# Kernel optimization log

Hardware: AMD Instinct MI355X
Metric: run time of the kernel (lower is better)

## Reference

```python
import jax, jax.numpy as jnp
import numpy as np

E = 8          # num_experts
TOP_K = 2      # num_selects
D = 2048       # hidden_size
F_E = 8192 // E  # per-expert intermediate size
EPS = 1e-6
SCALE = E / TOP_K


def setup_inputs() -> dict:
    key = jax.random.key(0)
    ks = jax.random.split(key, 6)
    B, S = 2, 2048
    std = 0.02
    return {
        "hidden_states": jax.random.normal(ks[0], (B, S, D), jnp.float32),
        "router_w": jax.random.normal(ks[1], (E, D), jnp.float32) * std,   # Linear(D->E).weight
        "norm_w": jnp.ones((D,), jnp.float32),                               # RMSNorm weight
        "gate_w": jax.random.normal(ks[2], (E, D, F_E), jnp.float32) * std,  # per-expert gate_proj
        "up_w": jax.random.normal(ks[3], (E, D, F_E), jnp.float32) * std,    # per-expert up_proj
        "down_w": jax.random.normal(ks[4], (E, F_E, D), jnp.float32) * std,  # per-expert down_proj
    }


def reference(hidden_states, router_w, norm_w, gate_w, up_w, down_w):
    B, S, Dm = hidden_states.shape
    T = B * S
    flat = hidden_states.reshape(T, Dm)

    # RMSNorm (fp32 math) used ONLY for the router input
    xf = flat.astype(jnp.float32)
    var = jnp.mean(xf * xf, axis=-1, keepdims=True)
    router_in = norm_w * (xf * jax.lax.rsqrt(var + EPS)).astype(flat.dtype)

    # Router: softmax over experts, top-k, renormalize
    logits = router_in @ router_w.T                    # [T, E]
    probs = jax.nn.softmax(logits, axis=-1)
    topw, topi = jax.lax.top_k(probs, TOP_K)           # [T, k]
    topw = topw / jnp.sum(topw, axis=-1, keepdims=True)

    # Dense combine weights: zero for non-selected (token, expert) pairs,
    # so the dense expert evaluation below matches the masked gather/scatter math.
    cw = jnp.zeros((T, E), flat.dtype).at[jnp.arange(T)[:, None], topi].add(topw)

    # Experts receive the RAW flat hidden (not the normalized router input)
    g = jnp.einsum('td,edf->tef', flat, gate_w)        # [T, E, F_E]
    u = jnp.einsum('td,edf->tef', flat, up_w)
    a = jax.nn.silu(g) * u
    expert_out = jnp.einsum('tef,efd->ted', a, down_w) # [T, E, D]

    y = jnp.einsum('ted,te->td', expert_out, cw) * SCALE
    return y.reshape(B, S, Dm)
```

## Files before the change

### kernel.cpp

```cpp
#include <hip/hip_runtime.h>
#include <hip/hip_bf16.h>


#define TOK 4096
#define DIM 2048
#define NE 8
#define FE 1024
#define SCALE_F 4.0f
#define BK 32

typedef __bf16 bf16x8 __attribute__((ext_vector_type(8)));
typedef __bf16 bf16x4 __attribute__((ext_vector_type(4)));
typedef float f32x4 __attribute__((ext_vector_type(4)));

__device__ __forceinline__ void gll16(const void* g, void* l) {
  __builtin_amdgcn_global_load_lds(
      (const __attribute__((address_space(1))) unsigned int*)g,
      (__attribute__((address_space(3))) unsigned int*)l, 16, 0, 0);
}

#define MFMA16(a, b, c) __builtin_amdgcn_mfma_f32_16x16x32_bf16((a), (b), (c), 0, 0, 0)
#define VMCNT4 asm volatile("s_waitcnt vmcnt(4)" ::: "memory")
#define VMCNT0 asm volatile("s_waitcnt vmcnt(0)" ::: "memory")
#define LGKM0  asm volatile("s_waitcnt lgkmcnt(0)" ::: "memory")
#define SCHED0 __builtin_amdgcn_sched_barrier(0)
#define BAR    __builtin_amdgcn_s_barrier()

__global__ __launch_bounds__(256) void k_fused_cvt_router(
    const float* __restrict__ x, const float* __restrict__ rw,
    const float* __restrict__ nwt, __bf16* __restrict__ xbf,
    int* __restrict__ topi, float* __restrict__ topw,
    const float* __restrict__ gw, const float* __restrict__ uw,
    const float* __restrict__ dwp, __bf16* __restrict__ gwt,
    __bf16* __restrict__ uwt, __bf16* __restrict__ dwt) {
  __shared__ __align__(16) __bf16 lt[128][136];
  int tid = threadIdx.x;

  if (blockIdx.x < TOK) {
    int t = blockIdx.x;
    const float* xr = x + (size_t)t * DIM;
    float ssq = 0.f;
    float pe[NE];
#pragma unroll
    for (int e = 0; e < NE; ++e) pe[e] = 0.f;

#pragma unroll
    for (int i = 0; i < 2; ++i) {
      int c4 = tid + i * 256;
      float4 v = ((const float4*)xr)[c4];
      int c = c4 * 4;
      bf16x4 b;
      b[0] = (__bf16)v.x; b[1] = (__bf16)v.y; b[2] = (__bf16)v.z; b[3] = (__bf16)v.w;
      *(bf16x4*)(xbf + (size_t)t * DIM + c) = b;
      float m0 = nwt[c + 0] * v.x, m1 = nwt[c + 1] * v.y;
      float m2 = nwt[c + 2] * v.z, m3 = nwt[c + 3] * v.w;
      ssq += v.x * v.x + v.y * v.y + v.z * v.z + v.w * v.w;
#pragma unroll
      for (int e = 0; e < NE; ++e) {
        float4 rv = ((const float4*)(rw + (size_t)e * DIM))[c4];
        pe[e] += m0 * rv.x + m1 * rv.y + m2 * rv.z + m3 * rv.w;
      }
    }
#pragma unroll
    for (int off = 32; off > 0; off >>= 1) {
      ssq += __shfl_down(ssq, off);
#pragma unroll
      for (int e = 0; e < NE; ++e) pe[e] += __shfl_down(pe[e], off);
    }
    float (*red)[NE + 1] = (float (*)[NE + 1])&lt[0][0];
    int wid = tid >> 6, lane = tid & 63;
    if (lane == 0) {
      red[wid][0] = ssq;
#pragma unroll
      for (int e = 0; e < NE; ++e) red[wid][1 + e] = pe[e];
    }
    __syncthreads();
    if (tid == 0) {
      float s = red[0][0] + red[1][0] + red[2][0] + red[3][0];
      float rs = rsqrtf(s / (float)DIM + 1e-6f);
      float l[NE];
#pragma unroll
      for (int e = 0; e < NE; ++e)
        l[e] = (red[0][1 + e] + red[1][1 + e] + red[2][1 + e] + red[3][1 + e]) * rs;
      int i1 = 0;
#pragma unroll
      for (int e = 1; e < NE; ++e) if (l[e] > l[i1]) i1 = e;
      int i2 = -1;
#pragma unroll
      for (int e = 0; e < NE; ++e) if (e != i1 && (i2 < 0 || l[e] > l[i2])) i2 = e;
      float e2 = __expf(l[i2] - l[i1]);
      float inv = 1.f / (1.f + e2);
      topi[2 * t] = i1; topi[2 * t + 1] = i2;
      topw[2 * t] = inv; topw[2 * t + 1] = e2 * inv;
    }
  } else {
    int bx = blockIdx.x - TOK;
    int m = bx >> 7;
    int tilex = bx & 127;
    int which = m >> 3, e = m & 7;
    const float* src; __bf16* dst; int K, N;
    if (which == 0)      { src = gw;  dst = gwt; K = DIM; N = FE; }
    else if (which == 1) { src = uw;  dst = uwt; K = DIM; N = FE; }
    else                 { src = dwp; dst = dwt; K = FE;  N = DIM; }
    src += (size_t)e * K * N;
    dst += (size_t)e * K * N;
    int tiles_n = N / 128;
    int k0 = (tilex / tiles_n) * 128, n0c = (tilex % tiles_n) * 128;

#pragma unroll
    for (int p = 0; p < 16; ++p) {
      int idx = tid + p * 256;
      int row = idx >> 5, c4 = idx & 31;
      float4 v = *(const float4*)(src + (size_t)(k0 + row) * N + n0c + c4 * 4);
      int cc = c4 * 4;
      lt[cc + 0][row] = (__bf16)v.x;
      lt[cc + 1][row] = (__bf16)v.y;
      lt[cc + 2][row] = (__bf16)v.z;
      lt[cc + 3][row] = (__bf16)v.w;
    }
    __syncthreads();
    int kblocks = K >> 5;
    int n_ = tid >> 2, kc = tid & 3;
#pragma unroll
    for (int q = 0; q < 8; ++q) {
      int bn = q >> 2, bk = q & 3;
      size_t blk = ((size_t)((n0c >> 6) + bn) * kblocks + (k0 >> 5) + bk) * 2048;
      bf16x8 w = *(const bf16x8*)&lt[bn * 64 + n_][bk * 32 + kc * 8];
      *(bf16x8*)(dst + blk + n_ * 32 + kc * 8) = w;
    }
  }
}

__global__ __launch_bounds__(256) void k_prefix_place(
    int* __restrict__ offsets, const int* __restrict__ topi,
    const float* __restrict__ topw, int* __restrict__ row_token,
    float* __restrict__ row_wt, int* __restrict__ invp) {
  __shared__ int hist[4][NE];
  __shared__ int lcur[NE];
  int tid = threadIdx.x, wid = tid >> 6;
  if (tid < 4 * NE) ((int*)hist)[tid] = 0;
  __syncthreads();
  for (int i = tid; i < 2 * TOK; i += 256)
    atomicAdd(&hist[wid][topi[i]], 1);
  __syncthreads();
  if (tid == 0) {
    int acc = 0;
    for (int e = 0; e < NE; ++e) {
      int c = hist[0][e] + hist[1][e] + hist[2][e] + hist[3][e];
      offsets[e] = acc;
      lcur[e] = acc;
      acc += c;
    }
    offsets[NE] = acc;
  }
  __syncthreads();
  for (int t = tid; t < TOK; t += 256) {
#pragma unroll
    for (int s = 0; s < 2; ++s) {
      int e = topi[2 * t + s];
      int pos = atomicAdd(&lcur[e], 1);
      row_token[pos] = t;
      row_wt[pos] = topw[2 * t + s] * SCALE_F;
      invp[2 * t + s] = pos;
    }
  }
}

__global__ __launch_bounds__(256) void k_combine(
    const __bf16* __restrict__ dbuf, const float* __restrict__ topw,
    const int* __restrict__ invp, float* __restrict__ out) {
  int t = blockIdx.x;
  int c = threadIdx.x * 8;
  int p0 = invp[2 * t], p1 = invp[2 * t + 1];
  float w0 = topw[2 * t] * SCALE_F, w1 = topw[2 * t + 1] * SCALE_F;
  bf16x8 a = *(const bf16x8*)(dbuf + (size_t)p0 * DIM + c);
  bf16x8 b = *(const bf16x8*)(dbuf + (size_t)p1 * DIM + c);
  float4 o0, o1;
  o0.x = w0 * (float)a[0] + w1 * (float)b[0];
  o0.y = w0 * (float)a[1] + w1 * (float)b[1];
  o0.z = w0 * (float)a[2] + w1 * (float)b[2];
  o0.w = w0 * (float)a[3] + w1 * (float)b[3];
  o1.x = w0 * (float)a[4] + w1 * (float)b[4];
  o1.y = w0 * (float)a[5] + w1 * (float)b[5];
  o1.z = w0 * (float)a[6] + w1 * (float)b[6];
  o1.w = w0 * (float)a[7] + w1 * (float)b[7];
  *(float4*)(out + (size_t)t * DIM + c) = o0;
  *(float4*)(out + (size_t)t * DIM + c + 4) = o1;
}


__global__ __launch_bounds__(256) void k_gateup16(
    const __bf16* __restrict__ xbf, const __bf16* __restrict__ gwt,
    const __bf16* __restrict__ uwt, const int* __restrict__ row_token,
    const int* __restrict__ offsets, __bf16* __restrict__ abuf) {
  int lin = blockIdx.x;
  int nw = (lin & 7) * 512 + (lin >> 3);
  int ytile = nw & 31, xt = (nw >> 5) & 15, e = nw >> 9;
  int row_start = offsets[e], row_end = offsets[e + 1];
  int tile_row = row_start + ytile * 128;
  if (tile_row >= row_end) return;
  int n0 = xt * 64;

  __shared__ __align__(16) __bf16 As0[128][BK], As1[128][BK];
  __shared__ __align__(16) __bf16 Bg0[64][BK],  Bg1[64][BK];
  __shared__ __align__(16) __bf16 Bu0[64][BK],  Bu1[64][BK];
  __shared__ int toks[128];

  int tid = threadIdx.x;
  if (tid < 128) {
    int r = tile_row + tid;
    toks[tid] = (r < row_end) ? row_token[r] : row_token[row_start];
  }
  __syncthreads();

  int wid = tid >> 6, lane = tid & 63;
  int lrow = lane >> 2;
  int lke = (((lane & 3) ^ ((lane >> 3) & 3)) * 8);
  int lks = (((lane >> 4) ^ ((lane >> 1) & 3)) * 8);

  const __bf16* pa0 = xbf + (size_t)toks[wid * 32 + lrow] * DIM + lke;
  const __bf16* pa1 = xbf + (size_t)toks[wid * 32 + 16 + lrow] * DIM + lke;
  const __bf16* pg = gwt + (size_t)e * FE * DIM + (size_t)xt * 64 * 2048 +
                     (wid * 16 + lrow) * 32 + lke;
  const __bf16* pu = uwt + (size_t)e * FE * DIM + (size_t)xt * 64 * 2048 +
                     (wid * 16 + lrow) * 32 + lke;

  f32x4 accg[4][2], accu[4][2];
#pragma unroll
  for (int i = 0; i < 4; ++i)
#pragma unroll
    for (int j = 0; j < 2; ++j) { accg[i][j] = (f32x4)0.f; accu[i][j] = (f32x4)0.f; }

  int lr = lane & 15;
  int wm = (wid >> 1) * 64, wn = (wid & 1) * 32;

  bf16x8 af0, af1, af2, af3, bgv0, bgv1, buv0, buv1;

#define GU_STAGE(AS, BG, BU)                                 \
  do {                                                       \
    gll16(pa0, (void*)&AS[wid * 32][0]);                     \
    gll16(pa1, (void*)&AS[wid * 32 + 16][0]);                \
    gll16(pg, (void*)&BG[wid * 16][0]);                      \
    gll16(pu, (void*)&BU[wid * 16][0]);                      \
    pa0 += BK; pa1 += BK; pg += 2048; pu += 2048;            \
  } while (0)

#define GU_LOAD(AS, BG, BU)                                  \
  do {                                                       \
    af0 = *(const bf16x8*)&AS[wm + lr][lks];                 \
    af1 = *(const bf16x8*)&AS[wm + 16 + lr][lks];            \
    af2 = *(const bf16x8*)&AS[wm + 32 + lr][lks];            \
    af3 = *(const bf16x8*)&AS[wm + 48 + lr][lks];            \
    bgv0 = *(const bf16x8*)&BG[wn + lr][lks];                \
    bgv1 = *(const bf16x8*)&BG[wn + 16 + lr][lks];           \
    buv0 = *(const bf16x8*)&BU[wn + lr][lks];                \
    buv1 = *(const bf16x8*)&BU[wn + 16 + lr][lks];           \
  } while (0)

#define GU_MFMA()                                            \
  do {                                                       \
    __builtin_amdgcn_s_setprio(1);                           \
    accg[0][0] = MFMA16(af0, bgv0, accg[0][0]);              \
    accg[0][1] = MFMA16(af0, bgv1, accg[0][1]);              \
    accu[0][0] = MFMA16(af0, buv0, accu[0][0]);              \
    accu[0][1] = MFMA16(af0, buv1, accu[0][1]);              \
    accg[1][0] = MFMA16(af1, bgv0, accg[1][0]);              \
    accg[1][1] = MFMA16(af1, bgv1, accg[1][1]);              \
    accu[1][0] = MFMA16(af1, buv0, accu[1][0]);              \
    accu[1][1] = MFMA16(af1, buv1, accu[1][1]);              \
    accg[2][0] = MFMA16(af2, bgv0, accg[2][0]);              \
    accg[2][1] = MFMA16(af2, bgv1, accg[2][1]);              \
    accu[2][0] = MFMA16(af2, buv0, accu[2][0]);              \
    accu[2][1] = MFMA16(af2, buv1, accu[2][1]);              \
    accg[3][0] = MFMA16(af3, bgv0, accg[3][0]);              \
    accg[3][1] = MFMA16(af3, bgv1, accg[3][1]);              \
    accu[3][0] = MFMA16(af3, buv0, accu[3][0]);              \
    accu[3][1] = MFMA16(af3, buv1, accu[3][1]);              \
    __builtin_amdgcn_s_setprio(0);                           \
  } while (0)

  GU_STAGE(As0, Bg0, Bu0);
  GU_STAGE(As1, Bg1, Bu1);
#pragma unroll 1
  for (int it = 0; it < 31; ++it) {
    VMCNT4; BAR;
    GU_LOAD(As0, Bg0, Bu0);
    LGKM0; SCHED0; BAR;
    GU_STAGE(As0, Bg0, Bu0);
    GU_MFMA();
    VMCNT4; BAR;
    GU_LOAD(As1, Bg1, Bu1);
    LGKM0; SCHED0; BAR;
    GU_STAGE(As1, Bg1, Bu1);
    GU_MFMA();
  }
  VMCNT4; BAR;
  GU_LOAD(As0, Bg0, Bu0);
  GU_MFMA();
  VMCNT0; BAR;
  GU_LOAD(As1, Bg1, Bu1);
  GU_MFMA();
#undef GU_STAGE
#undef GU_LOAD
#undef GU_MFMA

  int rowq = (lane >> 4) * 4;
  f32x4* ag = &accg[0][0];
  f32x4* au = &accu[0][0];
#pragma unroll
  for (int mi = 0; mi < 4; ++mi) {
#pragma unroll
    for (int ni = 0; ni < 2; ++ni) {
#pragma unroll
      for (int j = 0; j < 4; ++j) {
        int rg = tile_row + wm + mi * 16 + rowq + j;
        if (rg < row_end) {
          float g = ag[mi * 2 + ni][j], u = au[mi * 2 + ni][j];
          float sig = 1.f / (1.f + __expf(-g));
          abuf[(size_t)rg * FE + n0 + wn + ni * 16 + lr] = (__bf16)(g * sig * u);
        }
      }
    }
  }
}

__global__ __launch_bounds__(256) void k_down16(
    const __bf16* __restrict__ abuf, const __bf16* __restrict__ dwt,
    const int* __restrict__ offsets, __bf16* __restrict__ dbuf) {
  int lin = blockIdx.x;
  int nw = (lin & 7) * 512 + (lin >> 3);
  int ytile = nw & 31, xt = (nw >> 5) & 15, e = nw >> 9;
  int row_start = offsets[e], row_end = offsets[e + 1];
  int tile_row = row_start + ytile * 128;
  if (tile_row >= row_end) return;
  int n0 = xt * 128;

  __shared__ __align__(16) __bf16 As0[128][BK], As1[128][BK];
  __shared__ __align__(16) __bf16 Bs0[128][BK], Bs1[128][BK];

  int tid = threadIdx.x;
  int wid = tid >> 6, lane = tid & 63;
  int lrow = lane >> 2;
  int lke = (((lane & 3) ^ ((lane >> 3) & 3)) * 8);
  int lks = (((lane >> 4) ^ ((lane >> 1) & 3)) * 8);

  const __bf16* pa0 = abuf + (size_t)(tile_row + wid * 32 + lrow) * FE + lke;
  const __bf16* pa1 = pa0 + (size_t)16 * FE;
  const __bf16* pb0 = dwt + (size_t)e * DIM * FE +
                      ((size_t)(2 * xt + (wid >> 1)) * 32) * 2048 +
                      ((wid & 1) * 32 + lrow) * 32 + lke;
  const __bf16* pb1 = pb0 + 16 * 32;

  f32x4 acc[4][4];
#pragma unroll
  for (int i = 0; i < 4; ++i)
#pragma unroll
    for (int j = 0; j < 4; ++j) acc[i][j] = (f32x4)0.f;

  int lr = lane & 15;
  int wm = (wid >> 1) * 64, wn = (wid & 1) * 64;

  bf16x8 af0, af1, af2, af3, bb0, bb1, bb2, bb3;

#define DN_STAGE(AS, BS)                                     \
  do {                                                       \
    gll16(pa0, (void*)&AS[wid * 32][0]);                     \
    gll16(pa1, (void*)&AS[wid * 32 + 16][0]);                \
    gll16(pb0, (void*)&BS[wid * 32][0]);                     \
    gll16(pb1, (void*)&BS[wid * 32 + 16][0]);                \
    pa0 += BK; pa1 += BK; pb0 += 2048; pb1 += 2048;          \
  } while (0)

#define DN_LOAD(AS, BS)                                      \
  do {                                                       \
    af0 = *(const bf16x8*)&AS[wm + lr][lks];                 \
    af1 = *(const bf16x8*)&AS[wm + 16 + lr][lks];            \
    af2 = *(const bf16x8*)&AS[wm + 32 + lr][lks];            \
    af3 = *(const bf16x8*)&AS[wm + 48 + lr][lks];            \
    bb0 = *(const bf16x8*)&BS[wn + lr][lks];                 \
    bb1 = *(const bf16x8*)&BS[wn + 16 + lr][lks];            \
    bb2 = *(const bf16x8*)&BS[wn + 32 + lr][lks];            \
    bb3 = *(const bf16x8*)&BS[wn + 48 + lr][lks];            \
  } while (0)

#define DN_MFMA()                                            \
  do {                                                       \
    __builtin_amdgcn_s_setprio(1);                           \
    acc[0][0] = MFMA16(af0, bb0, acc[0][0]);                 \
    acc[1][0] = MFMA16(af1, bb0, acc[1][0]);                 \
    acc[2][0] = MFMA16(af2, bb0, acc[2][0]);                 \
    acc[3][0] = MFMA16(af3, bb0, acc[3][0]);                 \
    acc[0][1] = MFMA16(af0, bb1, acc[0][1]);                 \
    acc[1][1] = MFMA16(af1, bb1, acc[1][1]);                 \
    acc[2][1] = MFMA16(af2, bb1, acc[2][1]);                 \
    acc[3][1] = MFMA16(af3, bb1, acc[3][1]);                 \
    acc[0][2] = MFMA16(af0, bb2, acc[0][2]);                 \
    acc[1][2] = MFMA16(af1, bb2, acc[1][2]);                 \
    acc[2][2] = MFMA16(af2, bb2, acc[2][2]);                 \
    acc[3][2] = MFMA16(af3, bb2, acc[3][2]);                 \
    acc[0][3] = MFMA16(af0, bb3, acc[0][3]);                 \
    acc[1][3] = MFMA16(af1, bb3, acc[1][3]);                 \
    acc[2][3] = MFMA16(af2, bb3, acc[2][3]);                 \
    acc[3][3] = MFMA16(af3, bb3, acc[3][3]);                 \
    __builtin_amdgcn_s_setprio(0);                           \
  } while (0)

  DN_STAGE(As0, Bs0);
  DN_STAGE(As1, Bs1);
#pragma unroll 1
  for (int it = 0; it < 15; ++it) {
    VMCNT4; BAR;
    DN_LOAD(As0, Bs0);
    LGKM0; SCHED0; BAR;
    DN_STAGE(As0, Bs0);
    DN_MFMA();
    VMCNT4; BAR;
    DN_LOAD(As1, Bs1);
    LGKM0; SCHED0; BAR;
    DN_STAGE(As1, Bs1);
    DN_MFMA();
  }
  VMCNT4; BAR;
  DN_LOAD(As0, Bs0);
  DN_MFMA();
  VMCNT0; BAR;
  DN_LOAD(As1, Bs1);
  DN_MFMA();
#undef DN_STAGE
#undef DN_LOAD
#undef DN_MFMA

  int rowq = (lane >> 4) * 4;
#pragma unroll
  for (int mi = 0; mi < 4; ++mi) {
#pragma unroll
    for (int j = 0; j < 4; ++j) {
      int rg = tile_row + wm + mi * 16 + rowq + j;
      if (rg < row_end) {
#pragma unroll
        for (int ni = 0; ni < 4; ++ni) {
          dbuf[(size_t)rg * DIM + n0 + wn + ni * 16 + lr] = (__bf16)acc[mi][ni][j];
        }
      }
    }
  }
}


#define PAD 8
__global__ __launch_bounds__(256) void k_gateup_fb(
    const __bf16* __restrict__ xbf, const float* __restrict__ gw,
    const float* __restrict__ uw, const int* __restrict__ row_token,
    const int* __restrict__ offsets, __bf16* __restrict__ abuf) {
  int e = blockIdx.z;
  int row_start = offsets[e], row_end = offsets[e + 1];
  int tile_row = row_start + blockIdx.y * 128;
  if (tile_row >= row_end) return;
  int n0 = blockIdx.x * 128;

  __shared__ __align__(16) __bf16 As[128][BK + PAD];
  __shared__ __align__(16) __bf16 Bgs[128][BK + PAD];
  __shared__ __align__(16) __bf16 Bus[128][BK + PAD];
  __shared__ int toks[128];

  int tid = threadIdx.x;
  if (tid < 128) {
    int r = tile_row + tid;
    toks[tid] = (r < row_end) ? row_token[r] : row_token[row_start];
  }
  __syncthreads();

  f32x4 accg[4][4]; f32x4 accu[4][4];
#pragma unroll
  for (int i = 0; i < 4; ++i)
#pragma unroll
    for (int j = 0; j < 4; ++j) { accg[i][j] = (f32x4)0.f; accu[i][j] = (f32x4)0.f; }

  int wid = tid >> 6, lane = tid & 63;
  int wm = (wid >> 1) * 64, wn = (wid & 1) * 64;
  int lr = lane & 15, lk = (lane >> 4) * 8;

  const float* gbase = gw + (size_t)e * DIM * FE + n0;
  const float* ubase = uw + (size_t)e * DIM * FE + n0;
  int n4 = (tid & 31) * 4;
  int kb = tid >> 5;

  for (int k0 = 0; k0 < DIM; k0 += BK) {
#pragma unroll
    for (int p = 0; p < 2; ++p) {
      int g = tid + p * 256;
      int r = g >> 2, kk = (g & 3) * 8;
      *(bf16x8*)&As[r][kk] = *(const bf16x8*)(xbf + (size_t)toks[r] * DIM + k0 + kk);
    }
#pragma unroll
    for (int p = 0; p < 4; ++p) {
      int k = kb + p * 8;
      const float4 vg = *(const float4*)(gbase + (size_t)(k0 + k) * FE + n4);
      const float4 vu = *(const float4*)(ubase + (size_t)(k0 + k) * FE + n4);
      Bgs[n4 + 0][k] = (__bf16)vg.x; Bgs[n4 + 1][k] = (__bf16)vg.y;
      Bgs[n4 + 2][k] = (__bf16)vg.z; Bgs[n4 + 3][k] = (__bf16)vg.w;
      Bus[n4 + 0][k] = (__bf16)vu.x; Bus[n4 + 1][k] = (__bf16)vu.y;
      Bus[n4 + 2][k] = (__bf16)vu.z; Bus[n4 + 3][k] = (__bf16)vu.w;
    }
    __syncthreads();

    bf16x8 af[4];
#pragma unroll
    for (int mi = 0; mi < 4; ++mi)
      af[mi] = *(const bf16x8*)&As[wm + mi * 16 + lr][lk];
#pragma unroll
    for (int ni = 0; ni < 4; ++ni) {
      bf16x8 bg = *(const bf16x8*)&Bgs[wn + ni * 16 + lr][lk];
      bf16x8 bu = *(const bf16x8*)&Bus[wn + ni * 16 + lr][lk];
#pragma unroll
      for (int mi = 0; mi < 4; ++mi) {
        accg[mi][ni] = MFMA16(af[mi], bg, accg[mi][ni]);
        accu[mi][ni] = MFMA16(af[mi], bu, accu[mi][ni]);
      }
    }
    __syncthreads();
  }

  int rowq = (lane >> 4) * 4;
#pragma unroll
  for (int mi = 0; mi < 4; ++mi) {
#pragma unroll
    for (int ni = 0; ni < 4; ++ni) {
#pragma unroll
      for (int j = 0; j < 4; ++j) {
        int rg = tile_row + wm + mi * 16 + rowq + j;
        if (rg < row_end) {
          float g = accg[mi][ni][j], u = accu[mi][ni][j];
          float sig = 1.f / (1.f + __expf(-g));
          abuf[(size_t)rg * FE + n0 + wn + ni * 16 + lr] = (__bf16)(g * sig * u);
        }
      }
    }
  }
}

__global__ __launch_bounds__(256) void k_down_fb(
    const __bf16* __restrict__ abuf, const float* __restrict__ dw,
    const int* __restrict__ row_token, const float* __restrict__ row_wt,
    const int* __restrict__ offsets, float* __restrict__ out) {
  int e = blockIdx.z;
  int row_start = offsets[e], row_end = offsets[e + 1];
  int tile_row = row_start + blockIdx.y * 128;
  if (tile_row >= row_end) return;
  int n0 = blockIdx.x * 128;

  __shared__ __align__(16) __bf16 As[128][BK + PAD];
  __shared__ __align__(16) __bf16 Bs[128][BK + PAD];

  int tid = threadIdx.x;
  f32x4 acc[4][4];
#pragma unroll
  for (int i = 0; i < 4; ++i)
#pragma unroll
    for (int j = 0; j < 4; ++j) acc[i][j] = (f32x4)0.f;

  int wid = tid >> 6, lane = tid & 63;
  int wm = (wid >> 1) * 64, wn = (wid & 1) * 64;
  int lr = lane & 15, lk = (lane >> 4) * 8;

  const float* dbase = dw + (size_t)e * FE * DIM + n0;
  int n4 = (tid & 31) * 4;
  int kb = tid >> 5;

  for (int k0 = 0; k0 < FE; k0 += BK) {
#pragma unroll
    for (int p = 0; p < 2; ++p) {
      int g = tid + p * 256;
      int r = g >> 2, kk = (g & 3) * 8;
      *(bf16x8*)&As[r][kk] = *(const bf16x8*)(abuf + (size_t)(tile_row + r) * FE + k0 + kk);
    }
#pragma unroll
    for (int p = 0; p < 4; ++p) {
      int k = kb + p * 8;
      const float4 vb = *(const float4*)(dbase + (size_t)(k0 + k) * DIM + n4);
      Bs[n4 + 0][k] = (__bf16)vb.x; Bs[n4 + 1][k] = (__bf16)vb.y;
      Bs[n4 + 2][k] = (__bf16)vb.z; Bs[n4 + 3][k] = (__bf16)vb.w;
    }
    __syncthreads();

    bf16x8 af[4];
#pragma unroll
    for (int mi = 0; mi < 4; ++mi)
      af[mi] = *(const bf16x8*)&As[wm + mi * 16 + lr][lk];
#pragma unroll
    for (int ni = 0; ni < 4; ++ni) {
      bf16x8 bb = *(const bf16x8*)&Bs[wn + ni * 16 + lr][lk];
#pragma unroll
      for (int mi = 0; mi < 4; ++mi)
        acc[mi][ni] = MFMA16(af[mi], bb, acc[mi][ni]);
    }
    __syncthreads();
  }

  int rowq = (lane >> 4) * 4;
#pragma unroll
  for (int mi = 0; mi < 4; ++mi) {
#pragma unroll
    for (int j = 0; j < 4; ++j) {
      int rg = tile_row + wm + mi * 16 + rowq + j;
      if (rg < row_end) {
        int tok = row_token[rg];
        float w = row_wt[rg];
#pragma unroll
        for (int ni = 0; ni < 4; ++ni) {
          atomicAdd(&out[(size_t)tok * DIM + n0 + wn + ni * 16 + lr],
                    acc[mi][ni][j] * w);
        }
      }
    }
  }
}

extern "C" void kernel_launch(void* const* d_in, const int* in_sizes, int n_in,
                              void* d_out, int out_size, void* d_ws, size_t ws_size,
                              hipStream_t stream) {
  const float* x  = (const float*)d_in[0];
  const float* rw = (const float*)d_in[1];
  const float* nw = (const float*)d_in[2];
  const float* gw = (const float*)d_in[3];
  const float* uw = (const float*)d_in[4];
  const float* dwp= (const float*)d_in[5];
  float* out = (float*)d_out;

  char* p = (char*)d_ws;
  int* offsets   = (int*)(p + 64);
  int* topi      = (int*)(p + 256);
  float* topw    = (float*)(p + 256 + 32768);
  int* row_token = (int*)(p + 256 + 65536);
  float* row_wt  = (float*)(p + 256 + 98304);
  int* invp      = (int*)(p + 256 + 131072);
  __bf16* xbf    = (__bf16*)(p + 256 + 163840);
  __bf16* abuf   = xbf + (size_t)TOK * DIM;
  __bf16* gwt    = abuf + ((size_t)2 * TOK + 128) * FE;
  __bf16* uwt    = gwt + (size_t)NE * DIM * FE;
  __bf16* dwt    = uwt + (size_t)NE * DIM * FE;
  __bf16* dbuf   = gwt;

  size_t need = 256 + 163840 +
                ((size_t)TOK * DIM + ((size_t)2 * TOK + 128) * FE) * 2 +
                3 * (size_t)NE * DIM * FE * 2;
  bool fast = ws_size >= need;

  if (!fast)
    hipMemsetAsync(d_out, 0, (size_t)TOK * DIM * sizeof(float), stream);

  if (fast) {
    k_fused_cvt_router<<<TOK + 3072, 256, 0, stream>>>(
        x, rw, nw, xbf, topi, topw, gw, uw, dwp, gwt, uwt, dwt);
    k_prefix_place<<<1, 256, 0, stream>>>(offsets, topi, topw,
                                          row_token, row_wt, invp);
    k_gateup16<<<4096, 256, 0, stream>>>(xbf, gwt, uwt, row_token, offsets, abuf);
    k_down16<<<4096, 256, 0, stream>>>(abuf, dwt, offsets, dbuf);
    k_combine<<<TOK, 256, 0, stream>>>(dbuf, topw, invp, out);
  } else {
    k_fused_cvt_router<<<TOK, 256, 0, stream>>>(
        x, rw, nw, xbf, topi, topw, gw, uw, dwp, gwt, uwt, dwt);
    k_prefix_place<<<1, 256, 0, stream>>>(offsets, topi, topw,
                                          row_token, row_wt, invp);
    k_gateup_fb<<<dim3(FE / 128, 32, NE), 256, 0, stream>>>(xbf, gw, uw, row_token, offsets, abuf);
    k_down_fb<<<dim3(DIM / 128, 32, NE), 256, 0, stream>>>(abuf, dwp, row_token, row_wt, offsets, out);
  }
}
```

Measured before the change: 254.2 us.

## Load expert weight fragments directly into registers, bypassing LDS staging

The gate/up and down grouped GEMMs now read B (weight) MFMA fragments straight from global memory into registers, double-buffered across iterations, instead of staging them through LDS. Only the gathered activation tile still goes through LDS, and the vmcnt wait depth is raised to cover the extra in-flight register loads. This is meant to cut LDS traffic, LDS footprint and ds_read pressure. In exchange each wave loads its own B fragments with no sharing across waves, which raises global/L2 traffic and VGPR usage.

```diff
diff --git a/kernel.cpp b/kernel.cpp
--- a/kernel.cpp
+++ b/kernel.cpp
@@ -20,7 +20,7 @@
 }
 
 #define MFMA16(a, b, c) __builtin_amdgcn_mfma_f32_16x16x32_bf16((a), (b), (c), 0, 0, 0)
-#define VMCNT4 asm volatile("s_waitcnt vmcnt(4)" ::: "memory")
+#define VMCNT6 asm volatile("s_waitcnt vmcnt(6)" ::: "memory")
 #define VMCNT0 asm volatile("s_waitcnt vmcnt(0)" ::: "memory")
 #define LGKM0  asm volatile("s_waitcnt lgkmcnt(0)" ::: "memory")
 #define SCHED0 __builtin_amdgcn_sched_barrier(0)
@@ -189,7 +189,7 @@
 }
 
 
-__global__ __launch_bounds__(256) void k_gateup16(
+__global__ __launch_bounds__(256) void k_gateup18(
     const __bf16* __restrict__ xbf, const __bf16* __restrict__ gwt,
     const __bf16* __restrict__ uwt, const int* __restrict__ row_token,
     const int* __restrict__ offsets, __bf16* __restrict__ abuf) {
@@ -202,8 +202,6 @@
   int n0 = xt * 64;
 
   __shared__ __align__(16) __bf16 As0[128][BK], As1[128][BK];
-  __shared__ __align__(16) __bf16 Bg0[64][BK],  Bg1[64][BK];
-  __shared__ __align__(16) __bf16 Bu0[64][BK],  Bu1[64][BK];
   __shared__ int toks[128];
 
   int tid = threadIdx.x;
@@ -220,88 +218,102 @@
 
   const __bf16* pa0 = xbf + (size_t)toks[wid * 32 + lrow] * DIM + lke;
   const __bf16* pa1 = xbf + (size_t)toks[wid * 32 + 16 + lrow] * DIM + lke;
-  const __bf16* pg = gwt + (size_t)e * FE * DIM + (size_t)xt * 64 * 2048 +
-                     (wid * 16 + lrow) * 32 + lke;
-  const __bf16* pu = uwt + (size_t)e * FE * DIM + (size_t)xt * 64 * 2048 +
-                     (wid * 16 + lrow) * 32 + lke;
-
-  f32x4 accg[4][2], accu[4][2];
-#pragma unroll
-  for (int i = 0; i < 4; ++i)
-#pragma unroll
-    for (int j = 0; j < 2; ++j) { accg[i][j] = (f32x4)0.f; accu[i][j] = (f32x4)0.f; }
 
   int lr = lane & 15;
   int wm = (wid >> 1) * 64, wn = (wid & 1) * 32;
-
-  bf16x8 af0, af1, af2, af3, bgv0, bgv1, buv0, buv1;
-
-#define GU_STAGE(AS, BG, BU)                                 \
+  int chunk = (lane >> 4) * 8;
+
+  const __bf16* pgB = gwt + (size_t)e * FE * DIM + (size_t)xt * 64 * 2048 +
+                      (wn + lr) * 32 + chunk;
+  const __bf16* puB = uwt + (size_t)e * FE * DIM + (size_t)xt * 64 * 2048 +
+                      (wn + lr) * 32 + chunk;
+
+  f32x4 accg[4][2], accu[4][2];
+#pragma unroll
+  for (int i = 0; i < 4; ++i)
+#pragma unroll
+    for (int j = 0; j < 2; ++j) { accg[i][j] = (f32x4)0.f; accu[i][j] = (f32x4)0.f; }
+
+  bf16x8 af0, af1, af2, af3;
+  bf16x8 eg0, eg1, eu0, eu1;
+  bf16x8 og0, og1, ou0, ou1;
+
+#define GU_STAGE_A(AS)                                       \
   do {                                                       \
     gll16(pa0, (void*)&AS[wid * 32][0]);                     \
     gll16(pa1, (void*)&AS[wid * 32 + 16][0]);                \
-    gll16(pg, (void*)&BG[wid * 16][0]);                      \
-    gll16(pu, (void*)&BU[wid * 16][0]);                      \
-    pa0 += BK; pa1 += BK; pg += 2048; pu += 2048;            \
-  } while (0)
-
-#define GU_LOAD(AS, BG, BU)                                  \
+    pa0 += BK; pa1 += BK;                                    \
+  } while (0)
+
+#define GU_LOAD_B(G0, G1, U0, U1)                            \
+  do {                                                       \
+    G0 = *(const bf16x8*)pgB;                                \
+    G1 = *(const bf16x8*)(pgB + 512);                        \
+    U0 = *(const bf16x8*)puB;                                \
+    U1 = *(const bf16x8*)(puB + 512);                        \
+    pgB += 2048; puB += 2048;                                \
+  } while (0)
+
+#define GU_LOAD_A(AS)                                        \
   do {                                                       \
     af0 = *(const bf16x8*)&AS[wm + lr][lks];                 \
     af1 = *(const bf16x8*)&AS[wm + 16 + lr][lks];            \
     af2 = *(const bf16x8*)&AS[wm + 32 + lr][lks];            \
     af3 = *(const bf16x8*)&AS[wm + 48 + lr][lks];            \
-    bgv0 = *(const bf16x8*)&BG[wn + lr][lks];                \
-    bgv1 = *(const bf16x8*)&BG[wn + 16 + lr][lks];           \
-    buv0 = *(const bf16x8*)&BU[wn + lr][lks];                \
-    buv1 = *(const bf16x8*)&BU[wn + 16 + lr][lks];           \
-  } while (0)
-
-#define GU_MFMA()                                            \
+  } while (0)
+
+#define GU_MFMA(G0, G1, U0, U1)                              \
   do {                                                       \
     __builtin_amdgcn_s_setprio(1);                           \
-    accg[0][0] = MFMA16(af0, bgv0, accg[0][0]);              \
-    accg[0][1] = MFMA16(af0, bgv1, accg[0][1]);              \
-    accu[0][0] = MFMA16(af0, buv0, accu[0][0]);              \
-    accu[0][1] = MFMA16(af0, buv1, accu[0][1]);              \
-    accg[1][0] = MFMA16(af1, bgv0, accg[1][0]);              \
-    accg[1][1] = MFMA16(af1, bgv1, accg[1][1]);              \
-    accu[1][0] = MFMA16(af1, buv0, accu[1][0]);              \
-    accu[1][1] = MFMA16(af1, buv1, accu[1][1]);              \
-    accg[2][0] = MFMA16(af2, bgv0, accg[2][0]);              \
-    accg[2][1] = MFMA16(af2, bgv1, accg[2][1]);              \
-    accu[2][0] = MFMA16(af2, buv0, accu[2][0]);              \
-    accu[2][1] = MFMA16(af2, buv1, accu[2][1]);              \
-    accg[3][0] = MFMA16(af3, bgv0, accg[3][0]);              \
-    accg[3][1] = MFMA16(af3, bgv1, accg[3][1]);              \
-    accu[3][0] = MFMA16(af3, buv0, accu[3][0]);              \
-    accu[3][1] = MFMA16(af3, buv1, accu[3][1]);              \
+    accg[0][0] = MFMA16(af0, G0, accg[0][0]);                \
+    accg[0][1] = MFMA16(af0, G1, accg[0][1]);                \
+    accu[0][0] = MFMA16(af0, U0, accu[0][0]);                \
+    accu[0][1] = MFMA16(af0, U1, accu[0][1]);                \
+    accg[1][0] = MFMA16(af1, G0, accg[1][0]);                \
+    accg[1][1] = MFMA16(af1, G1, accg[1][1]);                \
+    accu[1][0] = MFMA16(af1, U0, accu[1][0]);                \
+    accu[1][1] = MFMA16(af1, U1, accu[1][1]);                \
+    accg[2][0] = MFMA16(af2, G0, accg[2][0]);                \
+    accg[2][1] = MFMA16(af2, G1, accg[2][1]);                \
+    accu[2][0] = MFMA16(af2, U0, accu[2][0]);                \
+    accu[2][1] = MFMA16(af2, U1, accu[2][1]);                \
+    accg[3][0] = MFMA16(af3, G0, accg[3][0]);                \
+    accg[3][1] = MFMA16(af3, G1, accg[3][1]);                \
+    accu[3][0] = MFMA16(af3, U0, accu[3][0]);                \
+    accu[3][1] = MFMA16(af3, U1, accu[3][1]);                \
     __builtin_amdgcn_s_setprio(0);                           \
   } while (0)
 
-  GU_STAGE(As0, Bg0, Bu0);
-  GU_STAGE(As1, Bg1, Bu1);
+  GU_STAGE_A(As0);
+  GU_LOAD_B(eg0, eg1, eu0, eu1);
+  GU_STAGE_A(As1);
+  GU_LOAD_B(og0, og1, ou0, ou1);
 #pragma unroll 1
   for (int it = 0; it < 31; ++it) {
-    VMCNT4; BAR;
-    GU_LOAD(As0, Bg0, Bu0);
+    VMCNT6; BAR;
+    GU_LOAD_A(As0);
     LGKM0; SCHED0; BAR;
-    GU_STAGE(As0, Bg0, Bu0);
-    GU_MFMA();
-    VMCNT4; BAR;
-    GU_LOAD(As1, Bg1, Bu1);
+    GU_STAGE_A(As0);
+    GU_MFMA(eg0, eg1, eu0, eu1);
+    GU_LOAD_B(eg0, eg1, eu0, eu1);
+    VMCNT6; BAR;
+    GU_LOAD_A(As1);
     LGKM0; SCHED0; BAR;
-    GU_STAGE(As1, Bg1, Bu1);
-    GU_MFMA();
-  }
-  VMCNT4; BAR;
-  GU_LOAD(As0, Bg0, Bu0);
-  GU_MFMA();
+    GU_STAGE_A(As1);
+    GU_MFMA(og0, og1, ou0, ou1);
+    GU_LOAD_B(og0, og1, ou0, ou1);
+  }
+  VMCNT6; BAR;
+  GU_LOAD_A(As0);
+  LGKM0; SCHED0;
+  GU_MFMA(eg0, eg1, eu0, eu1);
   VMCNT0; BAR;
-  GU_LOAD(As1, Bg1, Bu1);
-  GU_MFMA();
-#undef GU_STAGE
-#undef GU_LOAD
+  GU_LOAD_A(As1);
+  LGKM0; SCHED0;
+  GU_MFMA(og0, og1, ou0, ou1);
+#undef GU_STAGE_A
+#undef GU_LOAD_B
+#undef GU_LOAD_A
 #undef GU_MFMA
 
   int rowq = (lane >> 4) * 4;
@@ -324,7 +336,7 @@
   }
 }
 
-__global__ __launch_bounds__(256) void k_down16(
+__global__ __launch_bounds__(256) void k_down18(
     const __bf16* __restrict__ abuf, const __bf16* __restrict__ dwt,
     const int* __restrict__ offsets, __bf16* __restrict__ dbuf) {
   int lin = blockIdx.x;
@@ -336,7 +348,6 @@
   int n0 = xt * 128;
 
   __shared__ __align__(16) __bf16 As0[128][BK], As1[128][BK];
-  __shared__ __align__(16) __bf16 Bs0[128][BK], Bs1[128][BK];
 
   int tid = threadIdx.x;
   int wid = tid >> 6, lane = tid & 63;
@@ -346,88 +357,101 @@
 
   const __bf16* pa0 = abuf + (size_t)(tile_row + wid * 32 + lrow) * FE + lke;
   const __bf16* pa1 = pa0 + (size_t)16 * FE;
-  const __bf16* pb0 = dwt + (size_t)e * DIM * FE +
-                      ((size_t)(2 * xt + (wid >> 1)) * 32) * 2048 +
-                      ((wid & 1) * 32 + lrow) * 32 + lke;
-  const __bf16* pb1 = pb0 + 16 * 32;
-
-  f32x4 acc[4][4];
-#pragma unroll
-  for (int i = 0; i < 4; ++i)
-#pragma unroll
-    for (int j = 0; j < 4; ++j) acc[i][j] = (f32x4)0.f;
 
   int lr = lane & 15;
   int wm = (wid >> 1) * 64, wn = (wid & 1) * 64;
-
-  bf16x8 af0, af1, af2, af3, bb0, bb1, bb2, bb3;
-
-#define DN_STAGE(AS, BS)                                     \
+  int chunk = (lane >> 4) * 8;
+
+  const __bf16* pB = dwt + (size_t)e * DIM * FE +
+                     ((size_t)(2 * xt + (wid & 1)) * 32) * 2048 +
+                     lr * 32 + chunk;
+
+  f32x4 acc[4][4];
+#pragma unroll
+  for (int i = 0; i < 4; ++i)
+#pragma unroll
+    for (int j = 0; j < 4; ++j) acc[i][j] = (f32x4)0.f;
+
+  bf16x8 af0, af1, af2, af3;
+  bf16x8 eb0, eb1, eb2, eb3;
+  bf16x8 ob0, ob1, ob2, ob3;
+
+#define DN_STAGE_A(AS)                                       \
   do {                                                       \
     gll16(pa0, (void*)&AS[wid * 32][0]);                     \
     gll16(pa1, (void*)&AS[wid * 32 + 16][0]);                \
-    gll16(pb0, (void*)&BS[wid * 32][0]);                     \
-    gll16(pb1, (void*)&BS[wid * 32 + 16][0]);                \
-    pa0 += BK; pa1 += BK; pb0 += 2048; pb1 += 2048;          \
-  } while (0)
-
-#define DN_LOAD(AS, BS)                                      \
+    pa0 += BK; pa1 += BK;                                    \
+  } while (0)
+
+#define DN_LOAD_B(B0, B1, B2, B3)                            \
+  do {                                                       \
+    B0 = *(const bf16x8*)pB;                                 \
+    B1 = *(const bf16x8*)(pB + 512);                         \
+    B2 = *(const bf16x8*)(pB + 1024);                        \
+    B3 = *(const bf16x8*)(pB + 1536);                        \
+    pB += 2048;                                              \
+  } while (0)
+
+#define DN_LOAD_A(AS)                                        \
   do {                                                       \
     af0 = *(const bf16x8*)&AS[wm + lr][lks];                 \
     af1 = *(const bf16x8*)&AS[wm + 16 + lr][lks];            \
     af2 = *(const bf16x8*)&AS[wm + 32 + lr][lks];            \
     af3 = *(const bf16x8*)&AS[wm + 48 + lr][lks];            \
-    bb0 = *(const bf16x8*)&BS[wn + lr][lks];                 \
-    bb1 = *(const bf16x8*)&BS[wn + 16 + lr][lks];            \
-    bb2 = *(const bf16x8*)&BS[wn + 32 + lr][lks];            \
-    bb3 = *(const bf16x8*)&BS[wn + 48 + lr][lks];            \
-  } while (0)
-
-#define DN_MFMA()                                            \
+  } while (0)
+
+#define DN_MFMA(B0, B1, B2, B3)                              \
   do {                                                       \
     __builtin_amdgcn_s_setprio(1);                           \
-    acc[0][0] = MFMA16(af0, bb0, acc[0][0]);                 \
-    acc[1][0] = MFMA16(af1, bb0, acc[1][0]);                 \
-    acc[2][0] = MFMA16(af2, bb0, acc[2][0]);                 \
-    acc[3][0] = MFMA16(af3, bb0, acc[3][0]);                 \
-    acc[0][1] = MFMA16(af0, bb1, acc[0][1]);                 \
-    acc[1][1] = MFMA16(af1, bb1, acc[1][1]);                 \
-    acc[2][1] = MFMA16(af2, bb1, acc[2][1]);                 \
-    acc[3][1] = MFMA16(af3, bb1, acc[3][1]);                 \
-    acc[0][2] = MFMA16(af0, bb2, acc[0][2]);                 \
-    acc[1][2] = MFMA16(af1, bb2, acc[1][2]);                 \
-    acc[2][2] = MFMA16(af2, bb2, acc[2][2]);                 \
-    acc[3][2] = MFMA16(af3, bb2, acc[3][2]);                 \
-    acc[0][3] = MFMA16(af0, bb3, acc[0][3]);                 \
-    acc[1][3] = MFMA16(af1, bb3, acc[1][3]);                 \
-    acc[2][3] = MFMA16(af2, bb3, acc[2][3]);                 \
-    acc[3][3] = MFMA16(af3, bb3, acc[3][3]);                 \
+    acc[0][0] = MFMA16(af0, B0, acc[0][0]);                  \
+    acc[1][0] = MFMA16(af1, B0, acc[1][0]);                  \
+    acc[2][0] = MFMA16(af2, B0, acc[2][0]);                  \
+    acc[3][0] = MFMA16(af3, B0, acc[3][0]);                  \
+    acc[0][1] = MFMA16(af0, B1, acc[0][1]);                  \
+    acc[1][1] = MFMA16(af1, B1, acc[1][1]);                  \
+    acc[2][1] = MFMA16(af2, B1, acc[2][1]);                  \
+    acc[3][1] = MFMA16(af3, B1, acc[3][1]);                  \
+    acc[0][2] = MFMA16(af0, B2, acc[0][2]);                  \
+    acc[1][2] = MFMA16(af1, B2, acc[1][2]);                  \
+    acc[2][2] = MFMA16(af2, B2, acc[2][2]);                  \
+    acc[3][2] = MFMA16(af3, B2, acc[3][2]);                  \
+    acc[0][3] = MFMA16(af0, B3, acc[0][3]);                  \
+    acc[1][3] = MFMA16(af1, B3, acc[1][3]);                  \
+    acc[2][3] = MFMA16(af2, B3, acc[2][3]);                  \
+    acc[3][3] = MFMA16(af3, B3, acc[3][3]);                  \
     __builtin_amdgcn_s_setprio(0);                           \
   } while (0)
 
-  DN_STAGE(As0, Bs0);
-  DN_STAGE(As1, Bs1);
+  DN_STAGE_A(As0);
+  DN_LOAD_B(eb0, eb1, eb2, eb3);
+  DN_STAGE_A(As1);
+  DN_LOAD_B(ob0, ob1, ob2, ob3);
 #pragma unroll 1
   for (int it = 0; it < 15; ++it) {
-    VMCNT4; BAR;
-    DN_LOAD(As0, Bs0);
+    VMCNT6; BAR;
+    DN_LOAD_A(As0);
     LGKM0; SCHED0; BAR;
-    DN_STAGE(As0, Bs0);
-    DN_MFMA();
-    VMCNT4; BAR;
-    DN_LOAD(As1, Bs1);
+    DN_STAGE_A(As0);
+    DN_MFMA(eb0, eb1, eb2, eb3);
+    DN_LOAD_B(eb0, eb1, eb2, eb3);
+    VMCNT6; BAR;
+    DN_LOAD_A(As1);
     LGKM0; SCHED0; BAR;
-    DN_STAGE(As1, Bs1);
-    DN_MFMA();
-  }
-  VMCNT4; BAR;
-  DN_LOAD(As0, Bs0);
-  DN_MFMA();
+    DN_STAGE_A(As1);
+    DN_MFMA(ob0, ob1, ob2, ob3);
+    DN_LOAD_B(ob0, ob1, ob2, ob3);
+  }
+  VMCNT6; BAR;
+  DN_LOAD_A(As0);
+  LGKM0; SCHED0;
+  DN_MFMA(eb0, eb1, eb2, eb3);
   VMCNT0; BAR;
-  DN_LOAD(As1, Bs1);
-  DN_MFMA();
-#undef DN_STAGE
-#undef DN_LOAD
+  DN_LOAD_A(As1);
+  LGKM0; SCHED0;
+  DN_MFMA(ob0, ob1, ob2, ob3);
+#undef DN_STAGE_A
+#undef DN_LOAD_B
+#undef DN_LOAD_A
 #undef DN_MFMA
 
   int rowq = (lane >> 4) * 4;
@@ -654,8 +678,8 @@
         x, rw, nw, xbf, topi, topw, gw, uw, dwp, gwt, uwt, dwt);
     k_prefix_place<<<1, 256, 0, stream>>>(offsets, topi, topw,
                                           row_token, row_wt, invp);
-    k_gateup16<<<4096, 256, 0, stream>>>(xbf, gwt, uwt, row_token, offsets, abuf);
-    k_down16<<<4096, 256, 0, stream>>>(abuf, dwt, offsets, dbuf);
+    k_gateup18<<<4096, 256, 0, stream>>>(xbf, gwt, uwt, row_token, offsets, abuf);
+    k_down18<<<4096, 256, 0, stream>>>(abuf, dwt, offsets, dbuf);
     k_combine<<<TOK, 256, 0, stream>>>(dbuf, topw, invp, out);
   } else {
     k_fused_cvt_router<<<TOK, 256, 0, stream>>>(
```

New measurement: 313.2 us. 1.23x slower.
